# Kernel optimization log

Measured on AMD Instinct MI355X. Metric: run time of the kernel, lower is better.

## Reference

```python
import jax, jax.numpy as jnp
import numpy as np

N_NODES = 100000
N_EDGES = 400000
N_GRAPHS = 2000
NODE_F = 78
HID = 128


def gcn_conv(x, src, dst, W, b, n_nodes):
    # PyG GCNConv: h = X @ W; add self-loops; symmetric norm; scatter-add; + bias
    h = x @ W
    loop = jnp.arange(n_nodes, dtype=src.dtype)
    s = jnp.concatenate([src, loop])
    d = jnp.concatenate([dst, loop])
    deg = jax.ops.segment_sum(jnp.ones_like(d, dtype=h.dtype), d, num_segments=n_nodes)
    dinv = jax.lax.rsqrt(deg)  # deg >= 1 due to self-loops
    coef = dinv[s] * dinv[d]  # [E+N]
    msg = h[s] * coef[:, None]  # gather + scale
    out = jax.ops.segment_sum(msg, d, num_segments=n_nodes)
    return out + b


def setup_inputs() -> dict:
    key = jax.random.key(0)
    ks = jax.random.split(key, 16)
    x = jax.random.normal(ks[0], (N_NODES, NODE_F), dtype=jnp.float32)
    edge_index = jax.random.randint(ks[1], (2, N_EDGES), 0, N_NODES, dtype=jnp.int64)
    batch = jnp.sort(jax.random.randint(ks[2], (N_NODES,), 0, N_GRAPHS, dtype=jnp.int64))
    def lin(k, fi, fo):
        lim = 1.0 / np.sqrt(fi)
        kw, kb = jax.random.split(k)
        return (jax.random.uniform(kw, (fi, fo), jnp.float32, -lim, lim),
                jax.random.uniform(kb, (fo,), jnp.float32, -lim, lim))
    W1, b1 = lin(ks[3], NODE_F, HID)
    W2, b2 = lin(ks[4], HID, 2 * HID)
    W3, b3 = lin(ks[5], 2 * HID, HID)
    fw1, fb1 = lin(ks[6], HID, 64)
    fw2, fb2 = lin(ks[7], 64, 1)
    return {"x": x, "edge_index": edge_index, "batch": batch,
            "W1": W1, "b1": b1, "W2": W2, "b2": b2, "W3": W3, "b3": b3,
            "fw1": fw1, "fb1": fb1, "fw2": fw2, "fb2": fb2}


def reference(x, edge_index, batch, W1, b1, W2, b2, W3, b3, fw1, fb1, fw2, fb2):
    src, dst = edge_index[0], edge_index[1]
    h = jax.nn.relu(gcn_conv(x, src, dst, W1, b1, N_NODES))
    h = jax.nn.relu(gcn_conv(h, src, dst, W2, b2, N_NODES))
    h = jax.nn.relu(gcn_conv(h, src, dst, W3, b3, N_NODES))
    # global_mean_pool over graph ids
    sums = jax.ops.segment_sum(h, batch, num_segments=N_GRAPHS)
    cnts = jax.ops.segment_sum(jnp.ones((N_NODES,), h.dtype), batch, num_segments=N_GRAPHS)
    pooled = sums / jnp.maximum(cnts, 1.0)[:, None]
    h = jax.nn.relu(pooled @ fw1 + fb1)
    return h @ fw2 + fb2  # [N_GRAPHS, 1]
```

## Files before the change

kernel.cpp:

```cpp
#include <hip/hip_runtime.h>

#define N_NODES 100000
#define N_EDGES 400000
#define N_GRAPHS 2000
#define NODE_F 78
#define HID 128
#define PAD 32
#define SENT N_NODES

typedef __attribute__((ext_vector_type(8))) short short8v;
typedef __attribute__((ext_vector_type(4))) float f32x4;

__device__ __forceinline__ ushort f2bf(float f) {
    unsigned u = __float_as_uint(f);
    unsigned r = (u + 0x7FFFu + ((u >> 16) & 1u)) >> 16;
    return (ushort)r;
}
__device__ __forceinline__ float bf2f(ushort b) {
    return __uint_as_float(((unsigned)b) << 16);
}
__device__ __forceinline__ float2 bfx2(const ushort* p) {
    unsigned u = *reinterpret_cast<const unsigned*>(p);
    return make_float2(__uint_as_float(u << 16), __uint_as_float(u & 0xffff0000u));
}


__global__ void setup_k(int* __restrict__ cursor, int4* __restrict__ csr4,
                        ushort* __restrict__ xb, ushort* __restrict__ b1,
                        ushort* __restrict__ b3) {
    int i = blockIdx.x * blockDim.x + threadIdx.x;
    if (i < N_NODES * PAD / 4) csr4[i] = make_int4(SENT, SENT, SENT, SENT);
    if (i < N_NODES) cursor[i] = 0;
    if (i < 80) xb[(size_t)N_NODES * 80 + i] = 0;
    if (i < 128) {
        b1[(size_t)N_NODES * 128 + i] = 0;
        b3[(size_t)N_NODES * 128 + i] = 0;
    }
}

__global__ void fill_csr_k(const int* __restrict__ src, const int* __restrict__ dst,
                           int* __restrict__ cursor, int* __restrict__ csr) {
    int e = blockIdx.x * blockDim.x + threadIdx.x;
    if (e >= N_EDGES) return;
    int s = src[e], d = dst[e];
    int p = atomicAdd(&cursor[d], 1);
    if (p < PAD) csr[d * PAD + p] = s;
}

__global__ void dinv_k(const int* __restrict__ deg, float* __restrict__ dinv, int n) {
    int i = blockIdx.x * blockDim.x + threadIdx.x;
    if (i < n) dinv[i] = rsqrtf((float)deg[i] + 1.0f);
}


__global__ void x2bf_k(const float* __restrict__ x, const float* __restrict__ dinv,
                       ushort* __restrict__ xb) {
    int idx = blockIdx.x * blockDim.x + threadIdx.x;
    if (idx >= N_NODES * 80) return;
    int n = idx / 80, f = idx - n * 80;
    xb[idx] = (f < NODE_F) ? f2bf(x[(long long)n * NODE_F + f] * dinv[n]) : (ushort)0;
}


__global__ void prep_wt_k(const float* __restrict__ W, ushort* __restrict__ Wth,
                          int K, int N) {
    int idx = blockIdx.x * blockDim.x + threadIdx.x;
    if (idx >= N * 256) return;
    int n = idx >> 8, k = idx & 255;
    Wth[idx] = (k < K) ? f2bf(W[(long long)k * N + n]) : (ushort)0;
}


__global__ __launch_bounds__(256) void gemm_mfma_k(
        const float* __restrict__ A, int lda, int K, int M,
        const ushort* __restrict__ Wth, const float* __restrict__ bias,
        const float* __restrict__ dinv, ushort* __restrict__ C, int N) {
    __shared__ ushort Ah[128 * 64];
    __shared__ ushort Al[128 * 64];
    __shared__ ushort Bh[128 * 64];
    const int tid = threadIdx.x;
    const int w = tid >> 6, l = tid & 63;
    const int bm = blockIdx.x * 128;
    const int bn = blockIdx.y * 128;

    f32x4 acc[2][8];
    #pragma unroll
    for (int m = 0; m < 2; ++m)
        #pragma unroll
        for (int j = 0; j < 8; ++j)
            acc[m][j] = (f32x4){0.f, 0.f, 0.f, 0.f};

    for (int k0 = 0; k0 < K; k0 += 64) {
        __syncthreads();
        #pragma unroll
        for (int i = 0; i < 8; ++i) {
            int idx = tid + i * 256;
            int r = idx >> 4;
            int kq = (idx & 15) * 4;
            ushort4 h4, l4;
            if (k0 + kq < K) {
                int gr = bm + r; if (gr >= M) gr = M - 1;
                float4 v = *reinterpret_cast<const float4*>(&A[(long long)gr * lda + k0 + kq]);
                h4.x = f2bf(v.x); l4.x = f2bf(v.x - bf2f(h4.x));
                h4.y = f2bf(v.y); l4.y = f2bf(v.y - bf2f(h4.y));
                h4.z = f2bf(v.z); l4.z = f2bf(v.z - bf2f(h4.z));
                h4.w = f2bf(v.w); l4.w = f2bf(v.w - bf2f(h4.w));
            } else {
                h4 = (ushort4){0, 0, 0, 0};
                l4 = (ushort4){0, 0, 0, 0};
            }
            int e = r * 64 + ((kq >> 3) ^ (r & 7)) * 8 + (kq & 7);
            *reinterpret_cast<ushort4*>(&Ah[e]) = h4;
            *reinterpret_cast<ushort4*>(&Al[e]) = l4;
        }
        #pragma unroll
        for (int i = 0; i < 4; ++i) {
            int idx = tid + i * 256;
            int n = idx >> 3, s0 = idx & 7;
            long long g = (long long)(bn + n) * 256 + k0 + s0 * 8;
            short8v vh = *reinterpret_cast<const short8v*>(&Wth[g]);
            int e = n * 64 + (s0 ^ (n & 7)) * 8;
            *reinterpret_cast<short8v*>(&Bh[e]) = vh;
        }
        __syncthreads();
        #pragma unroll
        for (int ks = 0; ks < 2; ++ks) {
            short8v ah[2], al[2];
            #pragma unroll
            for (int m = 0; m < 2; ++m) {
                int r = w * 32 + m * 16 + (l & 15);
                int e = r * 64 + ((ks * 4 + (l >> 4)) ^ (r & 7)) * 8;
                ah[m] = *reinterpret_cast<const short8v*>(&Ah[e]);
                al[m] = *reinterpret_cast<const short8v*>(&Al[e]);
            }
            #pragma unroll
            for (int j = 0; j < 8; ++j) {
                int n = j * 16 + (l & 15);
                int e = n * 64 + ((ks * 4 + (l >> 4)) ^ (n & 7)) * 8;
                short8v bh = *reinterpret_cast<const short8v*>(&Bh[e]);
                #pragma unroll
                for (int m = 0; m < 2; ++m) {
                    acc[m][j] = __builtin_amdgcn_mfma_f32_16x16x32_bf16(ah[m], bh, acc[m][j], 0, 0, 0);
                    acc[m][j] = __builtin_amdgcn_mfma_f32_16x16x32_bf16(al[m], bh, acc[m][j], 0, 0, 0);
                }
            }
        }
    }

    float dv[2][4];
    #pragma unroll
    for (int m = 0; m < 2; ++m)
        #pragma unroll
        for (int rg = 0; rg < 4; ++rg) {
            int gr = bm + w * 32 + m * 16 + (l >> 4) * 4 + rg;
            dv[m][rg] = (gr < M) ? dinv[gr] : 0.f;
        }
    #pragma unroll
    for (int j = 0; j < 8; ++j) {
        int gc = bn + j * 16 + (l & 15);
        float bv = bias[gc];
        #pragma unroll
        for (int m = 0; m < 2; ++m) {
            #pragma unroll
            for (int rg = 0; rg < 4; ++rg) {
                int gr = bm + w * 32 + m * 16 + (l >> 4) * 4 + rg;
                if (gr < M)
                    C[(long long)gr * N + gc] = f2bf(fmaxf(acc[m][j][rg] + bv, 0.0f) * dv[m][rg]);
            }
        }
    }
}


__global__ __launch_bounds__(256) void gemm23_k(
        const float* __restrict__ A,
        const ushort* __restrict__ W2h, const float* __restrict__ b2,
        const ushort* __restrict__ W3h, const float* __restrict__ dinv,
        ushort* __restrict__ C, int M) {
    __shared__ ushort Ah[64 * 64];
    __shared__ ushort Al[64 * 64];
    __shared__ ushort Bh[128 * 64];
    const int tid = threadIdx.x;
    const int w = tid >> 6, l = tid & 63;
    const int bm = blockIdx.x * 64;

    f32x4 acc2[16];
    #pragma unroll
    for (int j = 0; j < 16; ++j) acc2[j] = (f32x4){0.f, 0.f, 0.f, 0.f};

    for (int k0 = 0; k0 < 128; k0 += 64) {
        __syncthreads();
        #pragma unroll
        for (int i = 0; i < 4; ++i) {
            int idx = tid + i * 256;
            int r = idx >> 4;
            int kq = (idx & 15) * 4;
            int gr = bm + r; if (gr >= M) gr = M - 1;
            float4 v = *reinterpret_cast<const float4*>(&A[(long long)gr * 128 + k0 + kq]);
            ushort4 h4, l4;
            h4.x = f2bf(v.x); l4.x = f2bf(v.x - bf2f(h4.x));
            h4.y = f2bf(v.y); l4.y = f2bf(v.y - bf2f(h4.y));
            h4.z = f2bf(v.z); l4.z = f2bf(v.z - bf2f(h4.z));
            h4.w = f2bf(v.w); l4.w = f2bf(v.w - bf2f(h4.w));
            int e = r * 64 + ((kq >> 3) ^ (r & 7)) * 8 + (kq & 7);
            *reinterpret_cast<ushort4*>(&Ah[e]) = h4;
            *reinterpret_cast<ushort4*>(&Al[e]) = l4;
        }
        #pragma unroll
        for (int nh = 0; nh < 2; ++nh) {
            if (nh) __syncthreads();
            #pragma unroll
            for (int i = 0; i < 4; ++i) {
                int idx = tid + i * 256;
                int n = idx >> 3, s0 = idx & 7;
                long long g = (long long)(nh * 128 + n) * 256 + k0 + s0 * 8;
                short8v vh = *reinterpret_cast<const short8v*>(&W2h[g]);
                int e = n * 64 + (s0 ^ (n & 7)) * 8;
                *reinterpret_cast<short8v*>(&Bh[e]) = vh;
            }
            __syncthreads();
            #pragma unroll
            for (int ks = 0; ks < 2; ++ks) {
                int r = w * 16 + (l & 15);
                int ea = r * 64 + ((ks * 4 + (l >> 4)) ^ (r & 7)) * 8;
                short8v ah = *reinterpret_cast<const short8v*>(&Ah[ea]);
                short8v al = *reinterpret_cast<const short8v*>(&Al[ea]);
                #pragma unroll
                for (int jl = 0; jl < 8; ++jl) {
                    int n = jl * 16 + (l & 15);
                    int e = n * 64 + ((ks * 4 + (l >> 4)) ^ (n & 7)) * 8;
                    short8v bh = *reinterpret_cast<const short8v*>(&Bh[e]);
                    int j = nh * 8 + jl;
                    acc2[j] = __builtin_amdgcn_mfma_f32_16x16x32_bf16(ah, bh, acc2[j], 0, 0, 0);
                    acc2[j] = __builtin_amdgcn_mfma_f32_16x16x32_bf16(al, bh, acc2[j], 0, 0, 0);
                }
            }
        }
    }

    f32x4 acc3[8];
    #pragma unroll
    for (int j = 0; j < 8; ++j) acc3[j] = (f32x4){0.f, 0.f, 0.f, 0.f};

    #pragma unroll
    for (int ch = 0; ch < 4; ++ch) {
        __syncthreads();
        #pragma unroll
        for (int jj = 0; jj < 4; ++jj) {
            int j = ch * 4 + jj;
            float bv = b2[j * 16 + (l & 15)];
            #pragma unroll
            for (int rg = 0; rg < 4; ++rg) {
                int r = w * 16 + (l >> 4) * 4 + rg;
                float v = fmaxf(acc2[j][rg] + bv, 0.f);
                ushort h = f2bf(v);
                ushort lo = f2bf(v - bf2f(h));
                int cl = jj * 16 + (l & 15);
                int e = r * 64 + ((cl >> 3) ^ (r & 7)) * 8 + (cl & 7);
                Ah[e] = h; Al[e] = lo;
            }
        }
        #pragma unroll
        for (int i = 0; i < 4; ++i) {
            int idx = tid + i * 256;
            int n = idx >> 3, s0 = idx & 7;
            long long g = (long long)n * 256 + ch * 64 + s0 * 8;
            short8v vh = *reinterpret_cast<const short8v*>(&W3h[g]);
            int e = n * 64 + (s0 ^ (n & 7)) * 8;
            *reinterpret_cast<short8v*>(&Bh[e]) = vh;
        }
        __syncthreads();
        #pragma unroll
        for (int ks = 0; ks < 2; ++ks) {
            int r = w * 16 + (l & 15);
            int ea = r * 64 + ((ks * 4 + (l >> 4)) ^ (r & 7)) * 8;
            short8v ah = *reinterpret_cast<const short8v*>(&Ah[ea]);
            short8v al = *reinterpret_cast<const short8v*>(&Al[ea]);
            #pragma unroll
            for (int j3 = 0; j3 < 8; ++j3) {
                int n = j3 * 16 + (l & 15);
                int e = n * 64 + ((ks * 4 + (l >> 4)) ^ (n & 7)) * 8;
                short8v bh = *reinterpret_cast<const short8v*>(&Bh[e]);
                acc3[j3] = __builtin_amdgcn_mfma_f32_16x16x32_bf16(ah, bh, acc3[j3], 0, 0, 0);
                acc3[j3] = __builtin_amdgcn_mfma_f32_16x16x32_bf16(al, bh, acc3[j3], 0, 0, 0);
            }
        }
    }

    float dv[4];
    #pragma unroll
    for (int rg = 0; rg < 4; ++rg) {
        int gr = bm + w * 16 + (l >> 4) * 4 + rg;
        dv[rg] = (gr < M) ? dinv[gr] : 0.f;
    }
    #pragma unroll
    for (int j = 0; j < 8; ++j) {
        int gc = j * 16 + (l & 15);
        #pragma unroll
        for (int rg = 0; rg < 4; ++rg) {
            int gr = bm + w * 16 + (l >> 4) * 4 + rg;
            if (gr < M) C[(long long)gr * 128 + gc] = f2bf(acc3[j][rg] * dv[rg]);
        }
    }
}


__global__ __launch_bounds__(256) void gather78_k(const ushort* __restrict__ Xb,
        const int* __restrict__ deg, const int* __restrict__ csr,
        const float* __restrict__ dinv, float* __restrict__ out) {
    int wid = (blockIdx.x * blockDim.x + threadIdx.x) >> 6;
    int lane = threadIdx.x & 63;
    if (wid >= N_NODES) return;
    float di = dinv[wid];
    float ax = 0.f, ay = 0.f;
    bool act = lane < 40;
    if (act) {
        float2 v = bfx2(&Xb[(size_t)wid * 80 + lane * 2]);
        ax = v.x; ay = v.y;
    }
    int d = deg[wid]; if (d > PAD) d = PAD;
    const int4* e4 = reinterpret_cast<const int4*>(csr + wid * PAD);
    for (int j0 = 0; j0 < d; j0 += 4) {
        int4 e = e4[j0 >> 2];
        if (act) {
            float2 v0 = bfx2(&Xb[(size_t)e.x * 80 + lane * 2]);
            float2 v1 = bfx2(&Xb[(size_t)e.y * 80 + lane * 2]);
            float2 v2 = bfx2(&Xb[(size_t)e.z * 80 + lane * 2]);
            float2 v3 = bfx2(&Xb[(size_t)e.w * 80 + lane * 2]);
            ax += v0.x + v1.x + v2.x + v3.x;
            ay += v0.y + v1.y + v2.y + v3.y;
        }
    }
    if (act)
        *reinterpret_cast<float2*>(&out[(size_t)wid * 80 + lane * 2]) = make_float2(ax * di, ay * di);
}

__global__ __launch_bounds__(256) void gather128_k(const ushort* __restrict__ A,
        const int* __restrict__ deg, const int* __restrict__ csr,
        const float* __restrict__ dinv, float* __restrict__ out) {
    int wid = (blockIdx.x * blockDim.x + threadIdx.x) >> 6;
    int lane = threadIdx.x & 63;
    if (wid >= N_NODES) return;
    float di = dinv[wid];
    float2 v = bfx2(&A[(size_t)wid * 128 + lane * 2]);
    float ax = v.x, ay = v.y;
    int d = deg[wid]; if (d > PAD) d = PAD;
    const int4* e4 = reinterpret_cast<const int4*>(csr + wid * PAD);
    for (int j0 = 0; j0 < d; j0 += 4) {
        int4 e = e4[j0 >> 2];
        float2 w0 = bfx2(&A[(size_t)e.x * 128 + lane * 2]);
        float2 w1 = bfx2(&A[(size_t)e.y * 128 + lane * 2]);
        float2 w2 = bfx2(&A[(size_t)e.z * 128 + lane * 2]);
        float2 w3 = bfx2(&A[(size_t)e.w * 128 + lane * 2]);
        ax += w0.x + w1.x + w2.x + w3.x;
        ay += w0.y + w1.y + w2.y + w3.y;
    }
    *reinterpret_cast<float2*>(&out[(size_t)wid * 128 + lane * 2]) = make_float2(ax * di, ay * di);
}


__global__ __launch_bounds__(512) void pool_head_k(
        const ushort* __restrict__ A,
        const int* __restrict__ deg, const int* __restrict__ csr,
        const float* __restrict__ dinv, const float* __restrict__ b3,
        const int* __restrict__ batch,
        const float* __restrict__ fw1, const float* __restrict__ fb1,
        const float* __restrict__ fw2, const float* __restrict__ fb2,
        float* __restrict__ out) {
    __shared__ float part[8][HID];
    __shared__ float ps[HID];
    const int g = blockIdx.x;
    const int w = threadIdx.x >> 6, lane = threadIdx.x & 63;

    int start, end;
    {
        int l = 0, h = N_NODES;
        while (l < h) { int m = (l + h) >> 1; if (batch[m] < g) l = m + 1; else h = m; }
        start = l;
        h = N_NODES;
        while (l < h) { int m = (l + h) >> 1; if (batch[m] < g + 1) l = m + 1; else h = m; }
        end = l;
    }

    float sx = 0.f, sy = 0.f;
    const float bx = b3[lane * 2], by = b3[lane * 2 + 1];
    for (int i = start + w; i < end; i += 8) {
        float di = dinv[i];
        float2 v = bfx2(&A[(size_t)i * 128 + lane * 2]);
        float ax = v.x, ay = v.y;
        int d = deg[i]; if (d > PAD) d = PAD;
        const int4* e4 = reinterpret_cast<const int4*>(csr + i * PAD);
        for (int j0 = 0; j0 < d; j0 += 4) {
            int4 e = e4[j0 >> 2];
            float2 w0 = bfx2(&A[(size_t)e.x * 128 + lane * 2]);
            float2 w1 = bfx2(&A[(size_t)e.y * 128 + lane * 2]);
            float2 w2 = bfx2(&A[(size_t)e.z * 128 + lane * 2]);
            float2 w3 = bfx2(&A[(size_t)e.w * 128 + lane * 2]);
            ax += w0.x + w1.x + w2.x + w3.x;
            ay += w0.y + w1.y + w2.y + w3.y;
        }
        sx += fmaxf(ax * di + bx, 0.f);
        sy += fmaxf(ay * di + by, 0.f);
    }
    part[w][lane * 2] = sx;
    part[w][lane * 2 + 1] = sy;
    __syncthreads();

    if (w == 0) {
        float inv = (end > start) ? 1.0f / (float)(end - start) : 0.0f;
        float s0 = 0.f, s1 = 0.f;
        #pragma unroll
        for (int q = 0; q < 8; ++q) {
            s0 += part[q][lane * 2];
            s1 += part[q][lane * 2 + 1];
        }
        ps[lane * 2] = s0 * inv;
        ps[lane * 2 + 1] = s1 * inv;
    }
    __syncthreads();

    if (w == 0) {
        float acc = fb1[lane];
        #pragma unroll 8
        for (int k = 0; k < HID; ++k) acc = fmaf(ps[k], fw1[k * 64 + lane], acc);
        float v = fmaxf(acc, 0.0f) * fw2[lane];
        #pragma unroll
        for (int off = 32; off > 0; off >>= 1) v += __shfl_down(v, off);
        if (lane == 0) out[g] = v + fb2[0];
    }
}


extern "C" void kernel_launch(void* const* d_in, const int* in_sizes, int n_in,
                              void* d_out, int out_size, void* d_ws, size_t ws_size,
                              hipStream_t stream) {
    const float* x     = (const float*)d_in[0];
    const int*   ei    = (const int*)d_in[1];
    const int*   batch = (const int*)d_in[2];
    const float* W1 = (const float*)d_in[3];
    const float* b1 = (const float*)d_in[4];
    const float* W2 = (const float*)d_in[5];
    const float* b2 = (const float*)d_in[6];
    const float* W3 = (const float*)d_in[7];
    const float* b3 = (const float*)d_in[8];
    const float* fw1 = (const float*)d_in[9];
    const float* fb1 = (const float*)d_in[10];
    const float* fw2 = (const float*)d_in[11];
    const float* fb2 = (const float*)d_in[12];
    float* out = (float*)d_out;

    const int* src = ei;
    const int* dst = ei + N_EDGES;

    char* p = (char*)d_ws;
    float*  dinv = (float*)p;  p += 100352 * 4;
    int*    cur  = (int*)p;    p += 100352 * 4;
    int*    csr  = (int*)p;    p += (size_t)N_NODES * PAD * 4;
    ushort* w1h  = (ushort*)p; p += 256 * 256 * 2;
    ushort* w2h  = (ushort*)p; p += 256 * 256 * 2;
    ushort* w3h  = (ushort*)p; p += 256 * 256 * 2;
    ushort* xb   = (ushort*)p; p += (size_t)(N_NODES + 1) * 80 * 2;
    float*  xpad = (float*)p;  p += (size_t)N_NODES * 80 * 4;
    ushort* buf1 = (ushort*)p; p += (size_t)(N_NODES + 1) * 128 * 2;
    float*  buf2 = (float*)p;  p += (size_t)N_NODES * 128 * 4;
    ushort* buf3 = (ushort*)p; p += (size_t)(N_NODES + 1) * 128 * 2;

    const int T = 256;
    const int gw = (N_NODES * 64 + T - 1) / T;

    setup_k<<<(N_NODES * PAD / 4 + T - 1) / T, T, 0, stream>>>(cur, (int4*)csr, xb, buf1, buf3);
    fill_csr_k<<<(N_EDGES + T - 1) / T, T, 0, stream>>>(src, dst, cur, csr);
    dinv_k<<<(N_NODES + T - 1) / T, T, 0, stream>>>(cur, dinv, N_NODES);
    x2bf_k<<<(N_NODES * 80 + T - 1) / T, T, 0, stream>>>(x, dinv, xb);

    prep_wt_k<<<(128 * 256 + T - 1) / T, T, 0, stream>>>(W1, w1h, NODE_F, 128);
    prep_wt_k<<<(256 * 256 + T - 1) / T, T, 0, stream>>>(W2, w2h, HID, 256);
    prep_wt_k<<<(128 * 256 + T - 1) / T, T, 0, stream>>>(W3, w3h, 2 * HID, 128);

    gather78_k<<<gw, T, 0, stream>>>(xb, cur, csr, dinv, xpad);
    gemm_mfma_k<<<dim3(782, 1), 256, 0, stream>>>(xpad, 80, 80, N_NODES, w1h, b1, dinv, buf1, 128);

    gather128_k<<<gw, T, 0, stream>>>(buf1, cur, csr, dinv, buf2);
    gemm23_k<<<1563, 256, 0, stream>>>(buf2, w2h, b2, w3h, dinv, buf3, N_NODES);

    pool_head_k<<<N_GRAPHS, 512, 0, stream>>>(buf3, cur, csr, dinv, b3, batch,
                                              fw1, fb1, fw2, fb2, out);
}
```

Measured before the change: 341.6 us.

## Store aggregated activations in bf16 and drop split-bf16 low-part MFMAs

The gather kernels now write their aggregated features as packed bf16 instead of fp32. The GEMMs therefore load bf16 directly and skip the hi/lo split, which halves the MFMA count and shrinks the LDS tiles. gemm23 also moves to 128-row tiles with 512 threads per block. This cuts intermediate memory traffic and compute, at the cost of lower accuracy from single-bf16 rounding of activations, which could exceed tolerance.

New measurement: 327.0 us. 4.3% less time.

```diff
diff --git a/kernel.cpp b/kernel.cpp
--- a/kernel.cpp
+++ b/kernel.cpp
@@ -22,6 +22,9 @@
 __device__ __forceinline__ float2 bfx2(const ushort* p) {
     unsigned u = *reinterpret_cast<const unsigned*>(p);
     return make_float2(__uint_as_float(u << 16), __uint_as_float(u & 0xffff0000u));
+}
+__device__ __forceinline__ unsigned packbf(float a, float b) {
+    return (unsigned)f2bf(a) | ((unsigned)f2bf(b) << 16);
 }
 
 
@@ -71,17 +74,15 @@
 }
 
 
-__global__ __launch_bounds__(256) void gemm_mfma_k(
-        const float* __restrict__ A, int lda, int K, int M,
+__global__ __launch_bounds__(256) void gemm1_k(
+        const ushort* __restrict__ A, int M,
         const ushort* __restrict__ Wth, const float* __restrict__ bias,
-        const float* __restrict__ dinv, ushort* __restrict__ C, int N) {
-    __shared__ ushort Ah[128 * 64];
-    __shared__ ushort Al[128 * 64];
+        const float* __restrict__ dinv, ushort* __restrict__ C) {
+    __shared__ ushort At[128 * 64];
     __shared__ ushort Bh[128 * 64];
     const int tid = threadIdx.x;
     const int w = tid >> 6, l = tid & 63;
     const int bm = blockIdx.x * 128;
-    const int bn = blockIdx.y * 128;
 
     f32x4 acc[2][8];
     #pragma unroll
@@ -90,59 +91,45 @@
         for (int j = 0; j < 8; ++j)
             acc[m][j] = (f32x4){0.f, 0.f, 0.f, 0.f};
 
-    for (int k0 = 0; k0 < K; k0 += 64) {
+    for (int k0 = 0; k0 < 128; k0 += 64) {
         __syncthreads();
         #pragma unroll
-        for (int i = 0; i < 8; ++i) {
+        for (int i = 0; i < 4; ++i) {
             int idx = tid + i * 256;
-            int r = idx >> 4;
-            int kq = (idx & 15) * 4;
-            ushort4 h4, l4;
-            if (k0 + kq < K) {
-                int gr = bm + r; if (gr >= M) gr = M - 1;
-                float4 v = *reinterpret_cast<const float4*>(&A[(long long)gr * lda + k0 + kq]);
-                h4.x = f2bf(v.x); l4.x = f2bf(v.x - bf2f(h4.x));
-                h4.y = f2bf(v.y); l4.y = f2bf(v.y - bf2f(h4.y));
-                h4.z = f2bf(v.z); l4.z = f2bf(v.z - bf2f(h4.z));
-                h4.w = f2bf(v.w); l4.w = f2bf(v.w - bf2f(h4.w));
-            } else {
-                h4 = (ushort4){0, 0, 0, 0};
-                l4 = (ushort4){0, 0, 0, 0};
-            }
-            int e = r * 64 + ((kq >> 3) ^ (r & 7)) * 8 + (kq & 7);
-            *reinterpret_cast<ushort4*>(&Ah[e]) = h4;
-            *reinterpret_cast<ushort4*>(&Al[e]) = l4;
+            int r = idx >> 3, s0 = idx & 7;
+            int gr = bm + r; if (gr >= M) gr = M - 1;
+            int kk = k0 + s0 * 8;
+            short8v v;
+            if (kk < 80) v = *reinterpret_cast<const short8v*>(&A[(size_t)gr * 80 + kk]);
+            else v = (short8v){0,0,0,0,0,0,0,0};
+            *reinterpret_cast<short8v*>(&At[r * 64 + (s0 ^ (r & 7)) * 8]) = v;
         }
         #pragma unroll
         for (int i = 0; i < 4; ++i) {
             int idx = tid + i * 256;
             int n = idx >> 3, s0 = idx & 7;
-            long long g = (long long)(bn + n) * 256 + k0 + s0 * 8;
-            short8v vh = *reinterpret_cast<const short8v*>(&Wth[g]);
-            int e = n * 64 + (s0 ^ (n & 7)) * 8;
-            *reinterpret_cast<short8v*>(&Bh[e]) = vh;
+            long long g = (long long)n * 256 + k0 + s0 * 8;
+            *reinterpret_cast<short8v*>(&Bh[n * 64 + (s0 ^ (n & 7)) * 8]) =
+                *reinterpret_cast<const short8v*>(&Wth[g]);
         }
         __syncthreads();
         #pragma unroll
         for (int ks = 0; ks < 2; ++ks) {
-            short8v ah[2], al[2];
+            short8v ah[2];
             #pragma unroll
             for (int m = 0; m < 2; ++m) {
                 int r = w * 32 + m * 16 + (l & 15);
-                int e = r * 64 + ((ks * 4 + (l >> 4)) ^ (r & 7)) * 8;
-                ah[m] = *reinterpret_cast<const short8v*>(&Ah[e]);
-                al[m] = *reinterpret_cast<const short8v*>(&Al[e]);
+                ah[m] = *reinterpret_cast<const short8v*>(
+                    &At[r * 64 + ((ks * 4 + (l >> 4)) ^ (r & 7)) * 8]);
             }
             #pragma unroll
             for (int j = 0; j < 8; ++j) {
                 int n = j * 16 + (l & 15);
-                int e = n * 64 + ((ks * 4 + (l >> 4)) ^ (n & 7)) * 8;
-                short8v bh = *reinterpret_cast<const short8v*>(&Bh[e]);
+                short8v bh = *reinterpret_cast<const short8v*>(
+                    &Bh[n * 64 + ((ks * 4 + (l >> 4)) ^ (n & 7)) * 8]);
                 #pragma unroll
-                for (int m = 0; m < 2; ++m) {
+                for (int m = 0; m < 2; ++m)
                     acc[m][j] = __builtin_amdgcn_mfma_f32_16x16x32_bf16(ah[m], bh, acc[m][j], 0, 0, 0);
-                    acc[m][j] = __builtin_amdgcn_mfma_f32_16x16x32_bf16(al[m], bh, acc[m][j], 0, 0, 0);
-                }
             }
         }
     }
@@ -157,7 +144,7 @@
         }
     #pragma unroll
     for (int j = 0; j < 8; ++j) {
-        int gc = bn + j * 16 + (l & 15);
+        int gc = j * 16 + (l & 15);
         float bv = bias[gc];
         #pragma unroll
         for (int m = 0; m < 2; ++m) {
@@ -165,24 +152,23 @@
             for (int rg = 0; rg < 4; ++rg) {
                 int gr = bm + w * 32 + m * 16 + (l >> 4) * 4 + rg;
                 if (gr < M)
-                    C[(long long)gr * N + gc] = f2bf(fmaxf(acc[m][j][rg] + bv, 0.0f) * dv[m][rg]);
-            }
-        }
-    }
-}
-
-
-__global__ __launch_bounds__(256) void gemm23_k(
-        const float* __restrict__ A,
+                    C[(size_t)gr * 128 + gc] = f2bf(fmaxf(acc[m][j][rg] + bv, 0.0f) * dv[m][rg]);
+            }
+        }
+    }
+}
+
+
+__global__ __launch_bounds__(512) void gemm23_k(
+        const ushort* __restrict__ A,
         const ushort* __restrict__ W2h, const float* __restrict__ b2,
         const ushort* __restrict__ W3h, const float* __restrict__ dinv,
         ushort* __restrict__ C, int M) {
-    __shared__ ushort Ah[64 * 64];
-    __shared__ ushort Al[64 * 64];
+    __shared__ ushort At[128 * 64];
     __shared__ ushort Bh[128 * 64];
     const int tid = threadIdx.x;
     const int w = tid >> 6, l = tid & 63;
-    const int bm = blockIdx.x * 64;
+    const int bm = blockIdx.x * 128;
 
     f32x4 acc2[16];
     #pragma unroll
@@ -191,48 +177,36 @@
     for (int k0 = 0; k0 < 128; k0 += 64) {
         __syncthreads();
         #pragma unroll
-        for (int i = 0; i < 4; ++i) {
-            int idx = tid + i * 256;
-            int r = idx >> 4;
-            int kq = (idx & 15) * 4;
+        for (int i = 0; i < 2; ++i) {
+            int idx = tid + i * 512;
+            int r = idx >> 3, s0 = idx & 7;
             int gr = bm + r; if (gr >= M) gr = M - 1;
-            float4 v = *reinterpret_cast<const float4*>(&A[(long long)gr * 128 + k0 + kq]);
-            ushort4 h4, l4;
-            h4.x = f2bf(v.x); l4.x = f2bf(v.x - bf2f(h4.x));
-            h4.y = f2bf(v.y); l4.y = f2bf(v.y - bf2f(h4.y));
-            h4.z = f2bf(v.z); l4.z = f2bf(v.z - bf2f(h4.z));
-            h4.w = f2bf(v.w); l4.w = f2bf(v.w - bf2f(h4.w));
-            int e = r * 64 + ((kq >> 3) ^ (r & 7)) * 8 + (kq & 7);
-            *reinterpret_cast<ushort4*>(&Ah[e]) = h4;
-            *reinterpret_cast<ushort4*>(&Al[e]) = l4;
+            *reinterpret_cast<short8v*>(&At[r * 64 + (s0 ^ (r & 7)) * 8]) =
+                *reinterpret_cast<const short8v*>(&A[(size_t)gr * 128 + k0 + s0 * 8]);
         }
         #pragma unroll
         for (int nh = 0; nh < 2; ++nh) {
             if (nh) __syncthreads();
             #pragma unroll
-            for (int i = 0; i < 4; ++i) {
-                int idx = tid + i * 256;
+            for (int i = 0; i < 2; ++i) {
+                int idx = tid + i * 512;
                 int n = idx >> 3, s0 = idx & 7;
                 long long g = (long long)(nh * 128 + n) * 256 + k0 + s0 * 8;
-                short8v vh = *reinterpret_cast<const short8v*>(&W2h[g]);
-                int e = n * 64 + (s0 ^ (n & 7)) * 8;
-                *reinterpret_cast<short8v*>(&Bh[e]) = vh;
+                *reinterpret_cast<short8v*>(&Bh[n * 64 + (s0 ^ (n & 7)) * 8]) =
+                    *reinterpret_cast<const short8v*>(&W2h[g]);
             }
             __syncthreads();
             #pragma unroll
             for (int ks = 0; ks < 2; ++ks) {
                 int r = w * 16 + (l & 15);
-                int ea = r * 64 + ((ks * 4 + (l >> 4)) ^ (r & 7)) * 8;
-                short8v ah = *reinterpret_cast<const short8v*>(&Ah[ea]);
-                short8v al = *reinterpret_cast<const short8v*>(&Al[ea]);
+                short8v ah = *reinterpret_cast<const short8v*>(
+                    &At[r * 64 + ((ks * 4 + (l >> 4)) ^ (r & 7)) * 8]);
                 #pragma unroll
                 for (int jl = 0; jl < 8; ++jl) {
                     int n = jl * 16 + (l & 15);
-                    int e = n * 64 + ((ks * 4 + (l >> 4)) ^ (n & 7)) * 8;
-                    short8v bh = *reinterpret_cast<const short8v*>(&Bh[e]);
-                    int j = nh * 8 + jl;
-                    acc2[j] = __builtin_amdgcn_mfma_f32_16x16x32_bf16(ah, bh, acc2[j], 0, 0, 0);
-                    acc2[j] = __builtin_amdgcn_mfma_f32_16x16x32_bf16(al, bh, acc2[j], 0, 0, 0);
+                    short8v bh = *reinterpret_cast<const short8v*>(
+                        &Bh[n * 64 + ((ks * 4 + (l >> 4)) ^ (n & 7)) * 8]);
+                    acc2[nh * 8 + jl] = __builtin_amdgcn_mfma_f32_16x16x32_bf16(ah, bh, acc2[nh * 8 + jl], 0, 0, 0);
                 }
             }
         }
@@ -252,37 +226,31 @@
             #pragma unroll
             for (int rg = 0; rg < 4; ++rg) {
                 int r = w * 16 + (l >> 4) * 4 + rg;
-                float v = fmaxf(acc2[j][rg] + bv, 0.f);
-                ushort h = f2bf(v);
-                ushort lo = f2bf(v - bf2f(h));
                 int cl = jj * 16 + (l & 15);
-                int e = r * 64 + ((cl >> 3) ^ (r & 7)) * 8 + (cl & 7);
-                Ah[e] = h; Al[e] = lo;
-            }
-        }
-        #pragma unroll
-        for (int i = 0; i < 4; ++i) {
-            int idx = tid + i * 256;
+                At[r * 64 + ((cl >> 3) ^ (r & 7)) * 8 + (cl & 7)] =
+                    f2bf(fmaxf(acc2[j][rg] + bv, 0.f));
+            }
+        }
+        #pragma unroll
+        for (int i = 0; i < 2; ++i) {
+            int idx = tid + i * 512;
             int n = idx >> 3, s0 = idx & 7;
             long long g = (long long)n * 256 + ch * 64 + s0 * 8;
-            short8v vh = *reinterpret_cast<const short8v*>(&W3h[g]);
-            int e = n * 64 + (s0 ^ (n & 7)) * 8;
-            *reinterpret_cast<short8v*>(&Bh[e]) = vh;
+            *reinterpret_cast<short8v*>(&Bh[n * 64 + (s0 ^ (n & 7)) * 8]) =
+                *reinterpret_cast<const short8v*>(&W3h[g]);
         }
         __syncthreads();
         #pragma unroll
         for (int ks = 0; ks < 2; ++ks) {
             int r = w * 16 + (l & 15);
-            int ea = r * 64 + ((ks * 4 + (l >> 4)) ^ (r & 7)) * 8;
-            short8v ah = *reinterpret_cast<const short8v*>(&Ah[ea]);
-            short8v al = *reinterpret_cast<const short8v*>(&Al[ea]);
+            short8v ah = *reinterpret_cast<const short8v*>(
+                &At[r * 64 + ((ks * 4 + (l >> 4)) ^ (r & 7)) * 8]);
             #pragma unroll
             for (int j3 = 0; j3 < 8; ++j3) {
                 int n = j3 * 16 + (l & 15);
-                int e = n * 64 + ((ks * 4 + (l >> 4)) ^ (n & 7)) * 8;
-                short8v bh = *reinterpret_cast<const short8v*>(&Bh[e]);
+                short8v bh = *reinterpret_cast<const short8v*>(
+                    &Bh[n * 64 + ((ks * 4 + (l >> 4)) ^ (n & 7)) * 8]);
                 acc3[j3] = __builtin_amdgcn_mfma_f32_16x16x32_bf16(ah, bh, acc3[j3], 0, 0, 0);
-                acc3[j3] = __builtin_amdgcn_mfma_f32_16x16x32_bf16(al, bh, acc3[j3], 0, 0, 0);
             }
         }
     }
@@ -299,7 +267,7 @@
         #pragma unroll
         for (int rg = 0; rg < 4; ++rg) {
             int gr = bm + w * 16 + (l >> 4) * 4 + rg;
-            if (gr < M) C[(long long)gr * 128 + gc] = f2bf(acc3[j][rg] * dv[rg]);
+            if (gr < M) C[(size_t)gr * 128 + gc] = f2bf(acc3[j][rg] * dv[rg]);
         }
     }
 }
@@ -307,7 +275,7 @@
 
 __global__ __launch_bounds__(256) void gather78_k(const ushort* __restrict__ Xb,
         const int* __restrict__ deg, const int* __restrict__ csr,
-        const float* __restrict__ dinv, float* __restrict__ out) {
+        const float* __restrict__ dinv, ushort* __restrict__ out) {
     int wid = (blockIdx.x * blockDim.x + threadIdx.x) >> 6;
     int lane = threadIdx.x & 63;
     if (wid >= N_NODES) return;
@@ -332,12 +300,12 @@
         }
     }
     if (act)
-        *reinterpret_cast<float2*>(&out[(size_t)wid * 80 + lane * 2]) = make_float2(ax * di, ay * di);
+        *reinterpret_cast<unsigned*>(&out[(size_t)wid * 80 + lane * 2]) = packbf(ax * di, ay * di);
 }
 
 __global__ __launch_bounds__(256) void gather128_k(const ushort* __restrict__ A,
         const int* __restrict__ deg, const int* __restrict__ csr,
-        const float* __restrict__ dinv, float* __restrict__ out) {
+        const float* __restrict__ dinv, ushort* __restrict__ out) {
     int wid = (blockIdx.x * blockDim.x + threadIdx.x) >> 6;
     int lane = threadIdx.x & 63;
     if (wid >= N_NODES) return;
@@ -355,7 +323,7 @@
         ax += w0.x + w1.x + w2.x + w3.x;
         ay += w0.y + w1.y + w2.y + w3.y;
     }
-    *reinterpret_cast<float2*>(&out[(size_t)wid * 128 + lane * 2]) = make_float2(ax * di, ay * di);
+    *reinterpret_cast<unsigned*>(&out[(size_t)wid * 128 + lane * 2]) = packbf(ax * di, ay * di);
 }
 
 
@@ -453,17 +421,17 @@
     const int* dst = ei + N_EDGES;
 
     char* p = (char*)d_ws;
-    float*  dinv = (float*)p;  p += 100352 * 4;
-    int*    cur  = (int*)p;    p += 100352 * 4;
-    int*    csr  = (int*)p;    p += (size_t)N_NODES * PAD * 4;
-    ushort* w1h  = (ushort*)p; p += 256 * 256 * 2;
-    ushort* w2h  = (ushort*)p; p += 256 * 256 * 2;
-    ushort* w3h  = (ushort*)p; p += 256 * 256 * 2;
-    ushort* xb   = (ushort*)p; p += (size_t)(N_NODES + 1) * 80 * 2;
-    float*  xpad = (float*)p;  p += (size_t)N_NODES * 80 * 4;
-    ushort* buf1 = (ushort*)p; p += (size_t)(N_NODES + 1) * 128 * 2;
-    float*  buf2 = (float*)p;  p += (size_t)N_NODES * 128 * 4;
-    ushort* buf3 = (ushort*)p; p += (size_t)(N_NODES + 1) * 128 * 2;
+    float*  dinv  = (float*)p;  p += 100352 * 4;
+    int*    cur   = (int*)p;    p += 100352 * 4;
+    int*    csr   = (int*)p;    p += (size_t)N_NODES * PAD * 4;
+    ushort* w1h   = (ushort*)p; p += 256 * 256 * 2;
+    ushort* w2h   = (ushort*)p; p += 256 * 256 * 2;
+    ushort* w3h   = (ushort*)p; p += 256 * 256 * 2;
+    ushort* xb    = (ushort*)p; p += (size_t)(N_NODES + 1) * 80 * 2;
+    ushort* xpadb = (ushort*)p; p += (size_t)N_NODES * 80 * 2;
+    ushort* buf1  = (ushort*)p; p += (size_t)(N_NODES + 1) * 128 * 2;
+    ushort* buf2  = (ushort*)p; p += (size_t)N_NODES * 128 * 2;
+    ushort* buf3  = (ushort*)p; p += (size_t)(N_NODES + 1) * 128 * 2;
 
     const int T = 256;
     const int gw = (N_NODES * 64 + T - 1) / T;
@@ -477,11 +445,11 @@
     prep_wt_k<<<(256 * 256 + T - 1) / T, T, 0, stream>>>(W2, w2h, HID, 256);
     prep_wt_k<<<(128 * 256 + T - 1) / T, T, 0, stream>>>(W3, w3h, 2 * HID, 128);
 
-    gather78_k<<<gw, T, 0, stream>>>(xb, cur, csr, dinv, xpad);
-    gemm_mfma_k<<<dim3(782, 1), 256, 0, stream>>>(xpad, 80, 80, N_NODES, w1h, b1, dinv, buf1, 128);
+    gather78_k<<<gw, T, 0, stream>>>(xb, cur, csr, dinv, xpadb);
+    gemm1_k<<<782, 256, 0, stream>>>(xpadb, N_NODES, w1h, b1, dinv, buf1);
 
     gather128_k<<<gw, T, 0, stream>>>(buf1, cur, csr, dinv, buf2);
-    gemm23_k<<<1563, 256, 0, stream>>>(buf2, w2h, b2, w3h, dinv, buf3, N_NODES);
+    gemm23_k<<<782, 512, 0, stream>>>(buf2, w2h, b2, w3h, dinv, buf3, N_NODES);
 
     pool_head_k<<<N_GRAPHS, 512, 0, stream>>>(buf3, cur, csr, dinv, b3, batch,
                                               fw1, fb1, fw2, fb2, out);
```
